# Optimization experiments

Measured on AMD Instinct MI355X. Metric: run time of the kernel, lower is better.

## Reference

```python
import jax, jax.numpy as jnp
import numpy as np

NUM_HEADS = 8
FOCUSING_FACTOR = 3
EPS = 1e-6


def _focus(x, f):
    # focusing: x**f, renormalized to keep the original L2 norm per token
    n = jnp.linalg.norm(x, axis=-1, keepdims=True)
    xp = x ** f
    return xp / jnp.linalg.norm(xp, axis=-1, keepdims=True) * n


def _split_heads(x, h):
    # b n (h c) -> (b h) n c
    b, n, C = x.shape
    return x.reshape(b, n, h, C // h).transpose(0, 2, 1, 3).reshape(b * h, n, C // h)


def setup_inputs() -> dict:
    key = jax.random.key(0)
    ks = jax.random.split(key, 9)
    B, Nq, Nkv, C = 8, 4096, 4096, 512
    query = jax.random.normal(ks[0], (B, Nq, C), jnp.float32)
    key_in = jax.random.normal(ks[1], (B, Nkv, C), jnp.float32)
    value = jax.random.normal(ks[2], (B, Nkv, C), jnp.float32)
    Wq = jax.random.normal(ks[3], (C, C), jnp.float32) * 0.02
    Wk = jax.random.normal(ks[4], (C, C), jnp.float32) * 0.02
    Wv = jax.random.normal(ks[5], (C, C), jnp.float32) * 0.02
    Wp = jax.random.normal(ks[6], (C, C), jnp.float32) * 0.02
    bp = jnp.zeros((C,), jnp.float32)
    scale = jax.random.normal(ks[7], (1, 1, C), jnp.float32) * 0.02
    return {"query": query, "key_in": key_in, "value": value,
            "Wq": Wq, "Wk": Wk, "Wv": Wv, "Wp": Wp, "bp": bp,
            "scale": scale, "H": 64, "W": 64}


def reference(query, key_in, value, Wq, Wk, Wv, Wp, bp, scale, H, W):
    B, N, C = query.shape
    h = NUM_HEADS
    # projections (qkv_bias=False)
    q = jax.nn.relu(query @ Wq) + EPS
    k = jax.nn.relu(key_in @ Wk) + EPS
    v = value @ Wv
    s = jax.nn.softplus(scale)  # [1,1,C]
    q = q / s
    k = k / s
    q = _focus(q, FOCUSING_FACTOR)
    k = _focus(k, FOCUSING_FACTOR)
    q = _split_heads(q, h)  # [(B h), N, c]
    k = _split_heads(k, h)
    v = _split_heads(v, h)
    # z-normalizer: 1 / (q . sum_j k_j)
    z = 1.0 / (jnp.einsum('bic,bc->bi', q, k.sum(axis=1)) + EPS)
    # O(n) kv-aggregation path (i*j*(c+d) > c*d*(i+j) for these shapes)
    kv = jnp.einsum('bjc,bjd->bcd', k, v)
    x = jnp.einsum('bic,bcd,bi->bid', q, kv, z)
    # (b h) n c -> b n (h c)
    x = x.reshape(B, h, N, C // h).transpose(0, 2, 1, 3).reshape(B, N, C)
    # note: dwc(v) feature_map in the original is dead code (never added to x)
    return x @ Wp + bp
```

## Files before the change

### kernel.cpp

```cpp
#include <hip/hip_runtime.h>
#include <hip/hip_bf16.h>
#include <math.h>

typedef __attribute__((ext_vector_type(8))) short short8;
typedef __attribute__((ext_vector_type(4))) float f32x4;

#define MFMA16x16x32(A,B,C) __builtin_amdgcn_mfma_f32_16x16x32_bf16((A),(B),(C),0,0,0)

__device__ __forceinline__ short f2b(float x) {
  __hip_bfloat16 h = __float2bfloat16(x);
  short s; __builtin_memcpy(&s, &h, 2); return s;
}
__device__ __forceinline__ float b2f(short s) {
  __hip_bfloat16 h; __builtin_memcpy(&h, &s, 2); return __bfloat162float(h);
}

__global__ __launch_bounds__(256)
void prep_kernel(const float* __restrict__ Wq, const float* __restrict__ Wk,
                 const float* __restrict__ Wv, const float* __restrict__ Wp,
                 const float* __restrict__ scale,
                 short* __restrict__ wpack, float* __restrict__ spls)
{
  const int b = blockIdx.x;
  const int t = threadIdx.x;
  if (b == 64) {
    for (int i = t; i < 512; i += 256) {
      float x = scale[i];
      spls[i] = (x > 20.f) ? x : log1pf(expf(x));
    }
    return;
  }
  const float* Ws[4] = {Wq, Wk, Wv, Wp};
  const int w = b >> 4, kf16 = b & 15;
  const float* W = Ws[w];
  short* dst = wpack + (size_t)w * (512 * 512);
  __shared__ short lds[32 * 512];
  for (int i = 0; i < 64; ++i) {
    int idx = i * 256 + t;
    int r = idx >> 9, c = idx & 511;
    lds[idx] = f2b(W[(size_t)(kf16 * 32 + r) * 512 + c]);
  }
  __syncthreads();
  for (int s = 0; s < 8; ++s) {
    int slot = s * 256 + t;
    int nf = slot >> 6, l = slot & 63;
    int n = nf * 16 + (l & 15);
    int k0 = 8 * (l >> 4);
    short8 v;
#pragma unroll
    for (int jj = 0; jj < 8; ++jj) v[jj] = lds[(k0 + jj) * 512 + n];
    *(short8*)(dst + ((size_t)(kf16 * 32 + nf) * 64 + l) * 8) = v;
  }
}

template<int MODE>
__global__ __launch_bounds__(512, 2)
void proj_kernel(const void* __restrict__ Xv, const short* __restrict__ wpk,
                 const float* __restrict__ spls, short* __restrict__ outp,
                 const float* __restrict__ bp, float* __restrict__ outf)
{
  __shared__ char smem[65536];
  __shared__ float pnorm[2][8][64];
  __shared__ float facs[64];
  short* tile = (short*)smem;
  const int t = threadIdx.x;
  const int lane = t & 63;
  const int wid = t >> 6;
  const int g = lane >> 4;
  const int cl = lane & 15;
  const int rb = blockIdx.x << 6;
  const int sr = t >> 3;
  const int sc = t & 7;

  const float* Xf = (const float*)Xv;
  const short* Xb = (const short*)Xv;
  const short8* wp8 = (const short8*)wpk;

  {
    char* dst = smem + sr * 272 + sc * 32;
    if (MODE < 3) {
      const float* src = Xf + (size_t)(rb + sr) * 512 + sc * 16;
      f32x4 a0 = *(const f32x4*)(src);
      f32x4 a1 = *(const f32x4*)(src + 4);
      f32x4 a2 = *(const f32x4*)(src + 8);
      f32x4 a3 = *(const f32x4*)(src + 12);
      short8 v0, v1;
#pragma unroll
      for (int j = 0; j < 4; ++j) {
        v0[j] = f2b(a0[j]); v0[4 + j] = f2b(a1[j]);
        v1[j] = f2b(a2[j]); v1[4 + j] = f2b(a3[j]);
      }
      *(short8*)dst = v0; *(short8*)(dst + 16) = v1;
    } else {
      const short* src = Xb + (size_t)(rb + sr) * 512 + sc * 16;
      *(short8*)dst = *(const short8*)src;
      *(short8*)(dst + 16) = *(const short8*)(src + 8);
    }
  }
  f32x4 zero4 = {0.f, 0.f, 0.f, 0.f};
  f32x4 acc[4][4];
#pragma unroll
  for (int rf = 0; rf < 4; ++rf)
#pragma unroll
    for (int cf = 0; cf < 4; ++cf) acc[rf][cf] = zero4;

  short8 bcur[4], bnxt[4];
#pragma unroll
  for (int cf = 0; cf < 4; ++cf)
    bcur[cf] = wp8[((size_t)(wid * 4 + cf)) * 64 + lane];
  __syncthreads();

#pragma unroll
  for (int s = 0; s < 4; ++s) {
    char* cur = smem + (s & 1) * 17408;
    char* nxt = smem + ((s + 1) & 1) * 17408;
    f32x4 rA0, rA1, rA2, rA3;
    short8 rB0, rB1;
    if (s < 3) {
      if (MODE < 3) {
        const float* src = Xf + (size_t)(rb + sr) * 512 + (s + 1) * 128 + sc * 16;
        rA0 = *(const f32x4*)(src);
        rA1 = *(const f32x4*)(src + 4);
        rA2 = *(const f32x4*)(src + 8);
        rA3 = *(const f32x4*)(src + 12);
      } else {
        const short* src = Xb + (size_t)(rb + sr) * 512 + (s + 1) * 128 + sc * 16;
        rB0 = *(const short8*)src;
        rB1 = *(const short8*)(src + 8);
      }
    }
#pragma unroll
    for (int kfl = 0; kfl < 4; ++kfl) {
      const int kf = s * 4 + kfl;
      if (kf < 15) {
#pragma unroll
        for (int cf = 0; cf < 4; ++cf)
          bnxt[cf] = wp8[((size_t)((kf + 1) * 32 + wid * 4 + cf)) * 64 + lane];
      }
      short8 af[4];
#pragma unroll
      for (int rf = 0; rf < 4; ++rf)
        af[rf] = *(const short8*)(cur + (rf * 16 + cl) * 272 + kfl * 64 + 16 * g);
#pragma unroll
      for (int rf = 0; rf < 4; ++rf)
#pragma unroll
        for (int cf = 0; cf < 4; ++cf)
          acc[rf][cf] = MFMA16x16x32(af[rf], bcur[cf], acc[rf][cf]);
      if (kf < 15) {
#pragma unroll
        for (int cf = 0; cf < 4; ++cf) bcur[cf] = bnxt[cf];
      }
    }
    if (s < 3) {
      char* dst = nxt + sr * 272 + sc * 32;
      short8 v0, v1;
      if (MODE < 3) {
#pragma unroll
        for (int j = 0; j < 4; ++j) {
          v0[j] = f2b(rA0[j]); v0[4 + j] = f2b(rA1[j]);
          v1[j] = f2b(rA2[j]); v1[4 + j] = f2b(rA3[j]);
        }
      } else { v0 = rB0; v1 = rB1; }
      *(short8*)dst = v0; *(short8*)(dst + 16) = v1;
      __syncthreads();
    }
  }

  if (MODE == 3) {
#pragma unroll
    for (int rf = 0; rf < 4; ++rf)
#pragma unroll
      for (int cf = 0; cf < 4; ++cf) {
        int c = wid * 64 + cf * 16 + cl;
        float bv = bp[c];
#pragma unroll
        for (int j = 0; j < 4; ++j)
          outf[(size_t)(rb + rf * 16 + 4 * g + j) * 512 + c] = acc[rf][cf][j] + bv;
      }
    return;
  }

  if (MODE < 2) {
    float sp_inv[4];
#pragma unroll
    for (int cf = 0; cf < 4; ++cf) sp_inv[cf] = 1.f / spls[wid * 64 + cf * 16 + cl];
    float p2[4][4], p6[4][4];
#pragma unroll
    for (int rf = 0; rf < 4; ++rf)
#pragma unroll
      for (int j = 0; j < 4; ++j) { p2[rf][j] = 0.f; p6[rf][j] = 0.f; }
#pragma unroll
    for (int rf = 0; rf < 4; ++rf)
#pragma unroll
      for (int cf = 0; cf < 4; ++cf)
#pragma unroll
        for (int j = 0; j < 4; ++j) {
          float v = acc[rf][cf][j];
          v = fmaxf(v, 0.f) + 1e-6f;
          v *= sp_inv[cf];
          acc[rf][cf][j] = v;
          float v2 = v * v;
          p2[rf][j] += v2;
          p6[rf][j] += v2 * v2 * v2;
        }
#pragma unroll
    for (int m = 1; m < 16; m <<= 1) {
#pragma unroll
      for (int rf = 0; rf < 4; ++rf)
#pragma unroll
        for (int j = 0; j < 4; ++j) {
          p2[rf][j] += __shfl_xor(p2[rf][j], m, 64);
          p6[rf][j] += __shfl_xor(p6[rf][j], m, 64);
        }
    }
    if (cl == 0) {
#pragma unroll
      for (int rf = 0; rf < 4; ++rf)
#pragma unroll
        for (int j = 0; j < 4; ++j) {
          pnorm[0][wid][rf * 16 + 4 * g + j] = p2[rf][j];
          pnorm[1][wid][rf * 16 + 4 * g + j] = p6[rf][j];
        }
    }
    __syncthreads();
    if (t < 64) {
      float a = 0.f, b = 0.f;
#pragma unroll
      for (int w = 0; w < 8; ++w) { a += pnorm[0][w][t]; b += pnorm[1][w][t]; }
      facs[t] = sqrtf(a / b);
    }
    __syncthreads();
    float fac[4][4];
#pragma unroll
    for (int rf = 0; rf < 4; ++rf)
#pragma unroll
      for (int j = 0; j < 4; ++j) fac[rf][j] = facs[rf * 16 + 4 * g + j];
#pragma unroll
    for (int rf = 0; rf < 4; ++rf)
#pragma unroll
      for (int cf = 0; cf < 4; ++cf)
#pragma unroll
        for (int j = 0; j < 4; ++j) {
          float v = acc[rf][cf][j];
          float o = v * v * v * fac[rf][j];
          int r = rf * 16 + 4 * g + j;
          int c = wid * 64 + cf * 16 + cl;
          int byteoff = (r * 1024 + c * 2) ^ ((r & 7) << 4);
          *(short*)((char*)tile + byteoff) = f2b(o);
        }
  } else {
    __syncthreads();
#pragma unroll
    for (int rf = 0; rf < 4; ++rf)
#pragma unroll
      for (int cf = 0; cf < 4; ++cf)
#pragma unroll
        for (int j = 0; j < 4; ++j) {
          int r = rf * 16 + 4 * g + j;
          int c = wid * 64 + cf * 16 + cl;
          int byteoff = (r * 1024 + c * 2) ^ ((r & 7) << 4);
          *(short*)((char*)tile + byteoff) = f2b(acc[rf][cf][j]);
        }
  }
  __syncthreads();

  if (MODE == 0) {
    const int r = t >> 3;
    const int c8 = t & 7;
#pragma unroll
    for (int s = 0; s < 8; ++s) {
      int ci = c8 + 8 * s;
      int byteoff = (r * 1024 + ci * 16) ^ ((r & 7) << 4);
      short8 v = *(const short8*)((const char*)tile + byteoff);
      *(short8*)(outp + (size_t)(rb + r) * 512 + ci * 8) = v;
    }
  } else {
    const int l = lane;
    const int batch = rb >> 12;
    const int jf_base = (rb & 4095) >> 5;
#pragma unroll
    for (int s = 0; s < 8; ++s) {
      int fidx = wid * 8 + s;
      int jf = fidx >> 5;
      int cf = fidx & 31;
      int c = cf * 16 + (l & 15);
      int j0 = jf * 32 + 8 * (l >> 4);
      short8 v;
#pragma unroll
      for (int jj = 0; jj < 8; ++jj) {
        int j = j0 + jj;
        int byteoff = (j * 1024 + c * 2) ^ ((j & 7) << 4);
        v[jj] = *(const short*)((const char*)tile + byteoff);
      }
      int bh = batch * 8 + (cf >> 2);
      int cfh = cf & 3;
      int jfg = jf_base + jf;
      *(short8*)(outp + (((size_t)(bh * 128 + jfg) * 4 + cfh) * 64 + l) * 8) = v;
    }
  }
}

__global__ __launch_bounds__(256)
void kv_kernel(const short* __restrict__ kpack, const short* __restrict__ vpack,
               float* __restrict__ pKV, float* __restrict__ pKS)
{
  __shared__ float red[4][64 * 64];
  __shared__ float ksacc[64];
  const int t = threadIdx.x;
  const int lane = t & 63;
  const int w = t >> 6;
  const int g = lane >> 4;
  const int cl = lane & 15;
  const int bh = blockIdx.x >> 3;
  const int sp = blockIdx.x & 7;
  if (t < 64) ksacc[t] = 0.f;
  __syncthreads();

  f32x4 zero4 = {0.f, 0.f, 0.f, 0.f};
  f32x4 acc[4][4];
#pragma unroll
  for (int df = 0; df < 4; ++df)
#pragma unroll
    for (int cf = 0; cf < 4; ++cf) acc[df][cf] = zero4;
  float ks[4] = {0.f, 0.f, 0.f, 0.f};
  const short8* kp = (const short8*)kpack;
  const short8* vp = (const short8*)vpack;

#pragma unroll
  for (int i = 0; i < 4; ++i) {
    int jfg = sp * 16 + w * 4 + i;
    size_t base = ((size_t)bh * 128 + jfg) * 4 * 64;
    short8 afr[4], bfr[4];
#pragma unroll
    for (int f = 0; f < 4; ++f) {
      afr[f] = vp[base + (size_t)f * 64 + lane];
      bfr[f] = kp[base + (size_t)f * 64 + lane];
    }
#pragma unroll
    for (int cf = 0; cf < 4; ++cf) {
      float s = 0.f;
#pragma unroll
      for (int jj = 0; jj < 8; ++jj) s += b2f(bfr[cf][jj]);
      ks[cf] += s;
    }
#pragma unroll
    for (int df = 0; df < 4; ++df)
#pragma unroll
      for (int cf = 0; cf < 4; ++cf)
        acc[df][cf] = MFMA16x16x32(afr[df], bfr[cf], acc[df][cf]);
  }

#pragma unroll
  for (int cf = 0; cf < 4; ++cf) {
    ks[cf] += __shfl_xor(ks[cf], 16, 64);
    ks[cf] += __shfl_xor(ks[cf], 32, 64);
  }
  if (lane < 16) {
#pragma unroll
    for (int cf = 0; cf < 4; ++cf) atomicAdd(&ksacc[cf * 16 + lane], ks[cf]);
  }

#pragma unroll
  for (int df = 0; df < 4; ++df)
#pragma unroll
    for (int cf = 0; cf < 4; ++cf)
#pragma unroll
      for (int j = 0; j < 4; ++j)
        red[w][(df * 16 + 4 * g + j) * 64 + cf * 16 + cl] = acc[df][cf][j];
  __syncthreads();

  float* dkv = pKV + (size_t)blockIdx.x * 4096;
  for (int i = t; i < 4096; i += 256)
    dkv[i] = red[0][i] + red[1][i] + red[2][i] + red[3][i];
  if (t < 64) pKS[(size_t)blockIdx.x * 64 + t] = ksacc[t];
}

__global__ __launch_bounds__(256)
void kv_reduce(const float* __restrict__ pKV, const float* __restrict__ pKS,
               short* __restrict__ kvT, float* __restrict__ ksum)
{
  const int bh = blockIdx.x;
  const int t = threadIdx.x;
  for (int i = t; i < 4096; i += 256) {
    float s = 0.f;
#pragma unroll
    for (int sp = 0; sp < 8; ++sp) s += pKV[(size_t)(bh * 8 + sp) * 4096 + i];
    kvT[(size_t)bh * 4096 + i] = f2b(s);
  }
  if (t < 64) {
    float s = 0.f;
#pragma unroll
    for (int sp = 0; sp < 8; ++sp) s += pKS[(size_t)(bh * 8 + sp) * 64 + t];
    ksum[bh * 64 + t] = s;
  }
}

__global__ __launch_bounds__(512)
void x_kernel(const short* __restrict__ qf, const short* __restrict__ kvT,
              const float* __restrict__ ksum, short* __restrict__ xout)
{
  __shared__ short xt[64 * 512];
  __shared__ float ksb[512];
  __shared__ float zb[64 * 8];
  const int t = threadIdx.x;
  const int lane = t & 63;
  const int wid = t >> 6;
  const int wr = wid >> 1;
  const int wc = wid & 1;
  const int g = lane >> 4;
  const int cl = lane & 15;
  const int rb = blockIdx.x << 6;
  const int batch = rb >> 12;

  ksb[t] = ksum[batch * 512 + t];
  __syncthreads();

  {
    int r = t >> 3, h = t & 7;
    const short8* qrow = (const short8*)(qf + (size_t)(rb + r) * 512 + h * 64);
    float d = 0.f;
#pragma unroll
    for (int c8 = 0; c8 < 8; ++c8) {
      short8 qv = qrow[c8];
#pragma unroll
      for (int jj = 0; jj < 8; ++jj) d += b2f(qv[jj]) * ksb[h * 64 + c8 * 8 + jj];
    }
    zb[r * 8 + h] = 1.f / (d + 1e-6f);
  }
  __syncthreads();

  f32x4 zero4 = {0.f, 0.f, 0.f, 0.f};
  f32x4 xacc[16];
#pragma unroll
  for (int i = 0; i < 16; ++i) xacc[i] = zero4;

  const short8* q8 = (const short8*)qf;
  const size_t qrowbase = (size_t)(rb + wr * 16 + cl) * 64;
#pragma unroll
  for (int hh = 0; hh < 4; ++hh) {
    int h = wc * 4 + hh;
    short8 af0 = q8[qrowbase + h * 8 + g];
    short8 af1 = q8[qrowbase + h * 8 + 4 + g];
    const short8* kv8 = (const short8*)kvT + ((size_t)(batch * 8 + h)) * 512;
#pragma unroll
    for (int nfl = 0; nfl < 4; ++nfl) {
      short8 b0 = kv8[(size_t)(nfl * 16 + cl) * 8 + g];
      short8 b1 = kv8[(size_t)(nfl * 16 + cl) * 8 + 4 + g];
      int nf = hh * 4 + nfl;
      xacc[nf] = MFMA16x16x32(af0, b0, xacc[nf]);
      xacc[nf] = MFMA16x16x32(af1, b1, xacc[nf]);
    }
  }
#pragma unroll
  for (int hh = 0; hh < 4; ++hh) {
    int h = wc * 4 + hh;
    float z4[4];
#pragma unroll
    for (int j = 0; j < 4; ++j) z4[j] = zb[(wr * 16 + 4 * g + j) * 8 + h];
#pragma unroll
    for (int nfl = 0; nfl < 4; ++nfl) {
      int nf = hh * 4 + nfl;
#pragma unroll
      for (int j = 0; j < 4; ++j) {
        float xv = xacc[nf][j] * z4[j];
        int r = wr * 16 + 4 * g + j;
        int c = wc * 256 + nf * 16 + cl;
        int byteoff = (r * 1024 + c * 2) ^ ((r & 7) << 4);
        *(short*)((char*)xt + byteoff) = f2b(xv);
      }
    }
  }
  __syncthreads();

  const int r = t >> 3;
  const int c8 = t & 7;
#pragma unroll
  for (int s = 0; s < 8; ++s) {
    int ci = c8 + 8 * s;
    int byteoff = (r * 1024 + ci * 16) ^ ((r & 7) << 4);
    short8 v = *(const short8*)((const char*)xt + byteoff);
    *(short8*)(xout + (size_t)(rb + r) * 512 + ci * 8) = v;
  }
}

extern "C" void kernel_launch(void* const* d_in, const int* in_sizes, int n_in,
                              void* d_out, int out_size, void* d_ws, size_t ws_size,
                              hipStream_t stream)
{
  const float* query  = (const float*)d_in[0];
  const float* key_in = (const float*)d_in[1];
  const float* value  = (const float*)d_in[2];
  const float* Wq     = (const float*)d_in[3];
  const float* Wk     = (const float*)d_in[4];
  const float* Wv     = (const float*)d_in[5];
  const float* Wp     = (const float*)d_in[6];
  const float* bp     = (const float*)d_in[7];
  const float* scale  = (const float*)d_in[8];
  float* out = (float*)d_out;

  char* ws = (char*)d_ws;
  size_t off = 0;
  auto alloc = [&](size_t bytes) -> void* {
    void* p = ws + off;
    off += (bytes + 255) & ~(size_t)255;
    return p;
  };
  float* spls  = (float*)alloc(512 * 4);
  short* wpack = (short*)alloc((size_t)4 * 512 * 512 * 2);
  short* qf    = (short*)alloc((size_t)32768 * 512 * 2);
  short* kpack = (short*)alloc((size_t)32768 * 512 * 2);
  short* vpack = (short*)alloc((size_t)32768 * 512 * 2);
  float* pKV   = (float*)alloc((size_t)512 * 4096 * 4);
  float* pKS   = (float*)alloc((size_t)512 * 64 * 4);
  short* kvT   = (short*)alloc((size_t)64 * 4096 * 2);
  float* ksum  = (float*)alloc((size_t)64 * 64 * 4);
  short* xbuf  = kpack;

  prep_kernel<<<65, 256, 0, stream>>>(Wq, Wk, Wv, Wp, scale, wpack, spls);
  proj_kernel<0><<<512, 512, 0, stream>>>(query,  wpack + (size_t)0 * 512 * 512, spls, qf,    nullptr, nullptr);
  proj_kernel<1><<<512, 512, 0, stream>>>(key_in, wpack + (size_t)1 * 512 * 512, spls, kpack, nullptr, nullptr);
  proj_kernel<2><<<512, 512, 0, stream>>>(value,  wpack + (size_t)2 * 512 * 512, spls, vpack, nullptr, nullptr);
  kv_kernel<<<512, 256, 0, stream>>>(kpack, vpack, pKV, pKS);
  kv_reduce<<<64, 256, 0, stream>>>(pKV, pKS, kvT, ksum);
  x_kernel<<<512, 512, 0, stream>>>(qf, kvT, ksum, xbuf);
  proj_kernel<3><<<512, 512, 0, stream>>>(xbuf, wpack + (size_t)3 * 512 * 512, spls, nullptr, bp, out);
}
```

Measured before the change: 212.3 us.

## Fuse Q/K/V projections into one launch with 128-row tiles and fragment-packed LDS

```diff
diff --git a/kernel.cpp b/kernel.cpp
--- a/kernel.cpp
+++ b/kernel.cpp
@@ -53,33 +53,41 @@
   }
 }
 
-template<int MODE>
-__global__ __launch_bounds__(512, 2)
-void proj_kernel(const void* __restrict__ Xv, const short* __restrict__ wpk,
-                 const float* __restrict__ spls, short* __restrict__ outp,
-                 const float* __restrict__ bp, float* __restrict__ outf)
+__global__ __launch_bounds__(1024, 4)
+void proj_big(const float* __restrict__ Aq, const float* __restrict__ Ak,
+              const float* __restrict__ Av, const short* __restrict__ Ax,
+              const short* __restrict__ wpack, const float* __restrict__ spls,
+              short* __restrict__ qf, short* __restrict__ kpack,
+              short* __restrict__ vpack, const float* __restrict__ bp,
+              float* __restrict__ outf, int mode_base)
 {
   __shared__ char smem[65536];
-  __shared__ float pnorm[2][8][64];
-  __shared__ float facs[64];
-  short* tile = (short*)smem;
+  __shared__ float pnorm[2][8][128];
+  __shared__ float facs[128];
+
   const int t = threadIdx.x;
   const int lane = t & 63;
   const int wid = t >> 6;
+  const int wr = wid >> 3;
+  const int wc = wid & 7;
   const int g = lane >> 4;
   const int cl = lane & 15;
-  const int rb = blockIdx.x << 6;
+  const int mode = mode_base + (blockIdx.x >> 8);
+  const int rb = (blockIdx.x & 255) << 7;
   const int sr = t >> 3;
   const int sc = t & 7;
 
-  const float* Xf = (const float*)Xv;
-  const short* Xb = (const short*)Xv;
-  const short8* wp8 = (const short8*)wpk;
+  const float* Af = (mode == 0) ? Aq : (mode == 1) ? Ak : Av;
+  const short8* wp8 = (const short8*)(wpack + (size_t)mode * (512 * 512));
+
+  const int stg_base = (((sc >> 1) * 8 + (sr >> 4)) * 64 + (sr & 15)) * 16;
+  const int stg_g0 = 16 * (2 * (sc & 1)) * 16;
+  const int stg_g1 = 16 * (2 * (sc & 1) + 1) * 16;
 
   {
-    char* dst = smem + sr * 272 + sc * 32;
-    if (MODE < 3) {
-      const float* src = Xf + (size_t)(rb + sr) * 512 + sc * 16;
+    char* dst = smem + stg_base;
+    if (mode < 3) {
+      const float* src = Af + (size_t)(rb + sr) * 512 + sc * 16;
       f32x4 a0 = *(const f32x4*)(src);
       f32x4 a1 = *(const f32x4*)(src + 4);
       f32x4 a2 = *(const f32x4*)(src + 8);
@@ -90,13 +98,14 @@
         v0[j] = f2b(a0[j]); v0[4 + j] = f2b(a1[j]);
         v1[j] = f2b(a2[j]); v1[4 + j] = f2b(a3[j]);
       }
-      *(short8*)dst = v0; *(short8*)(dst + 16) = v1;
+      *(short8*)(dst + stg_g0) = v0; *(short8*)(dst + stg_g1) = v1;
     } else {
-      const short* src = Xb + (size_t)(rb + sr) * 512 + sc * 16;
-      *(short8*)dst = *(const short8*)src;
-      *(short8*)(dst + 16) = *(const short8*)(src + 8);
-    }
-  }
+      const short* src = Ax + (size_t)(rb + sr) * 512 + sc * 16;
+      *(short8*)(dst + stg_g0) = *(const short8*)src;
+      *(short8*)(dst + stg_g1) = *(const short8*)(src + 8);
+    }
+  }
+
   f32x4 zero4 = {0.f, 0.f, 0.f, 0.f};
   f32x4 acc[4][4];
 #pragma unroll
@@ -107,24 +116,23 @@
   short8 bcur[4], bnxt[4];
 #pragma unroll
   for (int cf = 0; cf < 4; ++cf)
-    bcur[cf] = wp8[((size_t)(wid * 4 + cf)) * 64 + lane];
+    bcur[cf] = wp8[((size_t)(wc * 4 + cf)) * 64 + lane];
   __syncthreads();
 
 #pragma unroll
   for (int s = 0; s < 4; ++s) {
-    char* cur = smem + (s & 1) * 17408;
-    char* nxt = smem + ((s + 1) & 1) * 17408;
+    char* cur = smem + (s & 1) * 32768;
     f32x4 rA0, rA1, rA2, rA3;
     short8 rB0, rB1;
     if (s < 3) {
-      if (MODE < 3) {
-        const float* src = Xf + (size_t)(rb + sr) * 512 + (s + 1) * 128 + sc * 16;
+      if (mode < 3) {
+        const float* src = Af + (size_t)(rb + sr) * 512 + (s + 1) * 128 + sc * 16;
         rA0 = *(const f32x4*)(src);
         rA1 = *(const f32x4*)(src + 4);
         rA2 = *(const f32x4*)(src + 8);
         rA3 = *(const f32x4*)(src + 12);
       } else {
-        const short* src = Xb + (size_t)(rb + sr) * 512 + (s + 1) * 128 + sc * 16;
+        const short* src = Ax + (size_t)(rb + sr) * 512 + (s + 1) * 128 + sc * 16;
         rB0 = *(const short8*)src;
         rB1 = *(const short8*)(src + 8);
       }
@@ -135,95 +143,96 @@
       if (kf < 15) {
 #pragma unroll
         for (int cf = 0; cf < 4; ++cf)
-          bnxt[cf] = wp8[((size_t)((kf + 1) * 32 + wid * 4 + cf)) * 64 + lane];
+          bnxt[cf] = wp8[((size_t)((kf + 1) * 32 + wc * 4 + cf)) * 64 + lane];
       }
       short8 af[4];
 #pragma unroll
-      for (int rf = 0; rf < 4; ++rf)
-        af[rf] = *(const short8*)(cur + (rf * 16 + cl) * 272 + kfl * 64 + 16 * g);
-#pragma unroll
-      for (int rf = 0; rf < 4; ++rf)
+      for (int rfl = 0; rfl < 4; ++rfl)
+        af[rfl] = *(const short8*)(cur + ((kfl * 8 + wr * 4 + rfl) * 64 + lane) * 16);
+#pragma unroll
+      for (int rfl = 0; rfl < 4; ++rfl)
 #pragma unroll
         for (int cf = 0; cf < 4; ++cf)
-          acc[rf][cf] = MFMA16x16x32(af[rf], bcur[cf], acc[rf][cf]);
+          acc[rfl][cf] = MFMA16x16x32(af[rfl], bcur[cf], acc[rfl][cf]);
       if (kf < 15) {
 #pragma unroll
         for (int cf = 0; cf < 4; ++cf) bcur[cf] = bnxt[cf];
       }
     }
     if (s < 3) {
-      char* dst = nxt + sr * 272 + sc * 32;
+      char* dst = smem + ((s + 1) & 1) * 32768 + stg_base;
       short8 v0, v1;
-      if (MODE < 3) {
+      if (mode < 3) {
 #pragma unroll
         for (int j = 0; j < 4; ++j) {
           v0[j] = f2b(rA0[j]); v0[4 + j] = f2b(rA1[j]);
           v1[j] = f2b(rA2[j]); v1[4 + j] = f2b(rA3[j]);
         }
       } else { v0 = rB0; v1 = rB1; }
-      *(short8*)dst = v0; *(short8*)(dst + 16) = v1;
+      *(short8*)(dst + stg_g0) = v0; *(short8*)(dst + stg_g1) = v1;
       __syncthreads();
     }
   }
 
-  if (MODE == 3) {
-#pragma unroll
-    for (int rf = 0; rf < 4; ++rf)
+  if (mode == 3) {
+#pragma unroll
+    for (int rfl = 0; rfl < 4; ++rfl)
 #pragma unroll
       for (int cf = 0; cf < 4; ++cf) {
-        int c = wid * 64 + cf * 16 + cl;
+        int c = wc * 64 + cf * 16 + cl;
         float bv = bp[c];
 #pragma unroll
         for (int j = 0; j < 4; ++j)
-          outf[(size_t)(rb + rf * 16 + 4 * g + j) * 512 + c] = acc[rf][cf][j] + bv;
+          outf[(size_t)(rb + wr * 64 + rfl * 16 + 4 * g + j) * 512 + c] = acc[rfl][cf][j] + bv;
       }
     return;
   }
 
-  if (MODE < 2) {
+  if (mode < 2) {
     float sp_inv[4];
 #pragma unroll
-    for (int cf = 0; cf < 4; ++cf) sp_inv[cf] = 1.f / spls[wid * 64 + cf * 16 + cl];
+    for (int cf = 0; cf < 4; ++cf) sp_inv[cf] = 1.f / spls[wc * 64 + cf * 16 + cl];
     float p2[4][4], p6[4][4];
 #pragma unroll
-    for (int rf = 0; rf < 4; ++rf)
-#pragma unroll
-      for (int j = 0; j < 4; ++j) { p2[rf][j] = 0.f; p6[rf][j] = 0.f; }
-#pragma unroll
-    for (int rf = 0; rf < 4; ++rf)
+    for (int rfl = 0; rfl < 4; ++rfl)
+#pragma unroll
+      for (int j = 0; j < 4; ++j) { p2[rfl][j] = 0.f; p6[rfl][j] = 0.f; }
+#pragma unroll
+    for (int rfl = 0; rfl < 4; ++rfl)
 #pragma unroll
       for (int cf = 0; cf < 4; ++cf)
 #pragma unroll
         for (int j = 0; j < 4; ++j) {
-          float v = acc[rf][cf][j];
+          float v = acc[rfl][cf][j];
           v = fmaxf(v, 0.f) + 1e-6f;
           v *= sp_inv[cf];
-          acc[rf][cf][j] = v;
+          acc[rfl][cf][j] = v;
           float v2 = v * v;
-          p2[rf][j] += v2;
-          p6[rf][j] += v2 * v2 * v2;
+          p2[rfl][j] += v2;
+          p6[rfl][j] += v2 * v2 * v2;
         }
 #pragma unroll
     for (int m = 1; m < 16; m <<= 1) {
 #pragma unroll
-      for (int rf = 0; rf < 4; ++rf)
+      for (int rfl = 0; rfl < 4; ++rfl)
 #pragma unroll
         for (int j = 0; j < 4; ++j) {
-          p2[rf][j] += __shfl_xor(p2[rf][j], m, 64);
-          p6[rf][j] += __shfl_xor(p6[rf][j], m, 64);
+          p2[rfl][j] += __shfl_xor(p2[rfl][j], m, 64);
+          p6[rfl][j] += __shfl_xor(p6[rfl][j], m, 64);
         }
     }
     if (cl == 0) {
 #pragma unroll
-      for (int rf = 0; rf < 4; ++rf)
+      for (int rfl = 0; rfl < 4; ++rfl)
 #pragma unroll
         for (int j = 0; j < 4; ++j) {
-          pnorm[0][wid][rf * 16 + 4 * g + j] = p2[rf][j];
-          pnorm[1][wid][rf * 16 + 4 * g + j] = p6[rf][j];
+          int row = wr * 64 + rfl * 16 + 4 * g + j;
+          pnorm[0][wc][row] = p2[rfl][j];
+          pnorm[1][wc][row] = p6[rfl][j];
         }
     }
     __syncthreads();
-    if (t < 64) {
+    if (t < 128) {
       float a = 0.f, b = 0.f;
 #pragma unroll
       for (int w = 0; w < 8; ++w) { a += pnorm[0][w][t]; b += pnorm[1][w][t]; }
@@ -232,70 +241,71 @@
     __syncthreads();
     float fac[4][4];
 #pragma unroll
-    for (int rf = 0; rf < 4; ++rf)
-#pragma unroll
-      for (int j = 0; j < 4; ++j) fac[rf][j] = facs[rf * 16 + 4 * g + j];
-#pragma unroll
-    for (int rf = 0; rf < 4; ++rf)
+    for (int rfl = 0; rfl < 4; ++rfl)
+#pragma unroll
+      for (int j = 0; j < 4; ++j)
+        fac[rfl][j] = facs[wr * 64 + rfl * 16 + 4 * g + j];
+#pragma unroll
+    for (int rfl = 0; rfl < 4; ++rfl)
 #pragma unroll
       for (int cf = 0; cf < 4; ++cf)
 #pragma unroll
         for (int j = 0; j < 4; ++j) {
-          float v = acc[rf][cf][j];
-          float o = v * v * v * fac[rf][j];
-          int r = rf * 16 + 4 * g + j;
-          int c = wid * 64 + cf * 16 + cl;
-          int byteoff = (r * 1024 + c * 2) ^ ((r & 7) << 4);
-          *(short*)((char*)tile + byteoff) = f2b(o);
+          float v = acc[rfl][cf][j];
+          acc[rfl][cf][j] = v * v * v * fac[rfl][j];
         }
-  } else {
+  }
+
+  short* dstp = (mode == 0) ? qf : (mode == 1) ? kpack : vpack;
+  const int batch = rb >> 12;
+#pragma unroll
+  for (int pass = 0; pass < 2; ++pass) {
     __syncthreads();
-#pragma unroll
-    for (int rf = 0; rf < 4; ++rf)
-#pragma unroll
-      for (int cf = 0; cf < 4; ++cf)
-#pragma unroll
-        for (int j = 0; j < 4; ++j) {
-          int r = rf * 16 + 4 * g + j;
-          int c = wid * 64 + cf * 16 + cl;
-          int byteoff = (r * 1024 + c * 2) ^ ((r & 7) << 4);
-          *(short*)((char*)tile + byteoff) = f2b(acc[rf][cf][j]);
+    if (wr == pass) {
+#pragma unroll
+      for (int rfl = 0; rfl < 4; ++rfl)
+#pragma unroll
+        for (int cf = 0; cf < 4; ++cf)
+#pragma unroll
+          for (int j = 0; j < 4; ++j) {
+            int r = rfl * 16 + 4 * g + j;
+            int c = wc * 64 + cf * 16 + cl;
+            int byteoff = (r * 1024 + c * 2) ^ ((r & 7) << 4);
+            *(short*)(smem + byteoff) = f2b(acc[rfl][cf][j]);
+          }
+    }
+    __syncthreads();
+    if (mode == 0) {
+      const int r = t >> 4;
+      const int c16 = t & 15;
+#pragma unroll
+      for (int s2 = 0; s2 < 4; ++s2) {
+        int ci = c16 + 16 * s2;
+        int byteoff = (r * 1024 + ci * 16) ^ ((r & 7) << 4);
+        short8 v = *(const short8*)(smem + byteoff);
+        *(short8*)(dstp + (size_t)(rb + pass * 64 + r) * 512 + ci * 8) = v;
+      }
+    } else {
+      const int jf_base = ((rb & 4095) >> 5) + pass * 2;
+#pragma unroll
+      for (int s2 = 0; s2 < 4; ++s2) {
+        int fidx = wid * 4 + s2;
+        int jf = fidx >> 5;
+        int cf = fidx & 31;
+        int c = cf * 16 + (lane & 15);
+        int j0 = jf * 32 + 8 * (lane >> 4);
+        short8 v;
+#pragma unroll
+        for (int jj = 0; jj < 8; ++jj) {
+          int jrow = j0 + jj;
+          int byteoff = (jrow * 1024 + c * 2) ^ ((jrow & 7) << 4);
+          v[jj] = *(const short*)(smem + byteoff);
         }
-  }
-  __syncthreads();
-
-  if (MODE == 0) {
-    const int r = t >> 3;
-    const int c8 = t & 7;
-#pragma unroll
-    for (int s = 0; s < 8; ++s) {
-      int ci = c8 + 8 * s;
-      int byteoff = (r * 1024 + ci * 16) ^ ((r & 7) << 4);
-      short8 v = *(const short8*)((const char*)tile + byteoff);
-      *(short8*)(outp + (size_t)(rb + r) * 512 + ci * 8) = v;
-    }
-  } else {
-    const int l = lane;
-    const int batch = rb >> 12;
-    const int jf_base = (rb & 4095) >> 5;
-#pragma unroll
-    for (int s = 0; s < 8; ++s) {
-      int fidx = wid * 8 + s;
-      int jf = fidx >> 5;
-      int cf = fidx & 31;
-      int c = cf * 16 + (l & 15);
-      int j0 = jf * 32 + 8 * (l >> 4);
-      short8 v;
-#pragma unroll
-      for (int jj = 0; jj < 8; ++jj) {
-        int j = j0 + jj;
-        int byteoff = (j * 1024 + c * 2) ^ ((j & 7) << 4);
-        v[jj] = *(const short*)((const char*)tile + byteoff);
-      }
-      int bh = batch * 8 + (cf >> 2);
-      int cfh = cf & 3;
-      int jfg = jf_base + jf;
-      *(short8*)(outp + (((size_t)(bh * 128 + jfg) * 4 + cfh) * 64 + l) * 8) = v;
+        int bh = batch * 8 + (cf >> 2);
+        int cfh = cf & 3;
+        int jfg = jf_base + jf;
+        *(short8*)(dstp + (((size_t)(bh * 128 + jfg) * 4 + cfh) * 64 + lane) * 8) = v;
+      }
     }
   }
 }
@@ -517,11 +527,11 @@
   short* xbuf  = kpack;
 
   prep_kernel<<<65, 256, 0, stream>>>(Wq, Wk, Wv, Wp, scale, wpack, spls);
-  proj_kernel<0><<<512, 512, 0, stream>>>(query,  wpack + (size_t)0 * 512 * 512, spls, qf,    nullptr, nullptr);
-  proj_kernel<1><<<512, 512, 0, stream>>>(key_in, wpack + (size_t)1 * 512 * 512, spls, kpack, nullptr, nullptr);
-  proj_kernel<2><<<512, 512, 0, stream>>>(value,  wpack + (size_t)2 * 512 * 512, spls, vpack, nullptr, nullptr);
+  proj_big<<<768, 1024, 0, stream>>>(query, key_in, value, nullptr, wpack, spls,
+                                     qf, kpack, vpack, nullptr, nullptr, 0);
   kv_kernel<<<512, 256, 0, stream>>>(kpack, vpack, pKV, pKS);
   kv_reduce<<<64, 256, 0, stream>>>(pKV, pKS, kvT, ksum);
   x_kernel<<<512, 512, 0, stream>>>(qf, kvT, ksum, xbuf);
-  proj_kernel<3><<<512, 512, 0, stream>>>(xbuf, wpack + (size_t)3 * 512 * 512, spls, nullptr, bp, out);
-}
+  proj_big<<<256, 1024, 0, stream>>>(nullptr, nullptr, nullptr, xbuf, wpack, spls,
+                                     nullptr, nullptr, nullptr, bp, out, 3);
+}
```

Result: slower. 368.9 us (+73.7%).

## Merge Q/K/V projection launches into one grid and stagger K-slice order per block

Applied to the files above, without the earlier changes.

```diff
diff --git a/kernel.cpp b/kernel.cpp
--- a/kernel.cpp
+++ b/kernel.cpp
@@ -53,11 +53,13 @@
   }
 }
 
-template<int MODE>
 __global__ __launch_bounds__(512, 2)
-void proj_kernel(const void* __restrict__ Xv, const short* __restrict__ wpk,
-                 const float* __restrict__ spls, short* __restrict__ outp,
-                 const float* __restrict__ bp, float* __restrict__ outf)
+void proj_kernel(const float* __restrict__ Aq, const float* __restrict__ Ak,
+                 const float* __restrict__ Av, const short* __restrict__ Ax,
+                 const short* __restrict__ wpack, const float* __restrict__ spls,
+                 short* __restrict__ qf, short* __restrict__ kpk,
+                 short* __restrict__ vpk, const float* __restrict__ bp,
+                 float* __restrict__ outf, int mode_base)
 {
   __shared__ char smem[65536];
   __shared__ float pnorm[2][8][64];
@@ -68,18 +70,21 @@
   const int wid = t >> 6;
   const int g = lane >> 4;
   const int cl = lane & 15;
-  const int rb = blockIdx.x << 6;
+  const int bid = blockIdx.x;
+  const int mode = (mode_base == 3) ? 3 : (bid >> 9);
+  const int rb = (bid & 511) << 6;
   const int sr = t >> 3;
   const int sc = t & 7;
-
-  const float* Xf = (const float*)Xv;
-  const short* Xb = (const short*)Xv;
-  const short8* wp8 = (const short8*)wpk;
+  const int r1 = bid & 3;
+  const int r2 = (bid >> 2) & 3;
+
+  const float* Af = (mode == 0) ? Aq : (mode == 1) ? Ak : Av;
+  const short8* wp8 = (const short8*)(wpack + (size_t)mode * (512 * 512));
 
   {
     char* dst = smem + sr * 272 + sc * 32;
-    if (MODE < 3) {
-      const float* src = Xf + (size_t)(rb + sr) * 512 + sc * 16;
+    if (mode < 3) {
+      const float* src = Af + (size_t)(rb + sr) * 512 + r1 * 128 + sc * 16;
       f32x4 a0 = *(const f32x4*)(src);
       f32x4 a1 = *(const f32x4*)(src + 4);
       f32x4 a2 = *(const f32x4*)(src + 8);
@@ -92,7 +97,7 @@
       }
       *(short8*)dst = v0; *(short8*)(dst + 16) = v1;
     } else {
-      const short* src = Xb + (size_t)(rb + sr) * 512 + sc * 16;
+      const short* src = Ax + (size_t)(rb + sr) * 512 + r1 * 128 + sc * 16;
       *(short8*)dst = *(const short8*)src;
       *(short8*)(dst + 16) = *(const short8*)(src + 8);
     }
@@ -105,56 +110,63 @@
     for (int cf = 0; cf < 4; ++cf) acc[rf][cf] = zero4;
 
   short8 bcur[4], bnxt[4];
-#pragma unroll
-  for (int cf = 0; cf < 4; ++cf)
-    bcur[cf] = wp8[((size_t)(wid * 4 + cf)) * 64 + lane];
-  __syncthreads();
-
-#pragma unroll
-  for (int s = 0; s < 4; ++s) {
-    char* cur = smem + (s & 1) * 17408;
-    char* nxt = smem + ((s + 1) & 1) * 17408;
+  {
+    const int kf0 = r1 * 4 + r2;
+#pragma unroll
+    for (int cf = 0; cf < 4; ++cf)
+      bcur[cf] = wp8[((size_t)(kf0 * 32 + wid * 4 + cf)) * 64 + lane];
+  }
+  __syncthreads();
+
+#pragma unroll
+  for (int sl = 0; sl < 4; ++sl) {
+    const int s_phys = (sl + r1) & 3;
+    const int s_next = (s_phys + 1) & 3;
+    char* cur = smem + (sl & 1) * 17408;
     f32x4 rA0, rA1, rA2, rA3;
     short8 rB0, rB1;
-    if (s < 3) {
-      if (MODE < 3) {
-        const float* src = Xf + (size_t)(rb + sr) * 512 + (s + 1) * 128 + sc * 16;
+    if (sl < 3) {
+      if (mode < 3) {
+        const float* src = Af + (size_t)(rb + sr) * 512 + s_next * 128 + sc * 16;
         rA0 = *(const f32x4*)(src);
         rA1 = *(const f32x4*)(src + 4);
         rA2 = *(const f32x4*)(src + 8);
         rA3 = *(const f32x4*)(src + 12);
       } else {
-        const short* src = Xb + (size_t)(rb + sr) * 512 + (s + 1) * 128 + sc * 16;
+        const short* src = Ax + (size_t)(rb + sr) * 512 + s_next * 128 + sc * 16;
         rB0 = *(const short8*)src;
         rB1 = *(const short8*)(src + 8);
       }
     }
 #pragma unroll
-    for (int kfl = 0; kfl < 4; ++kfl) {
-      const int kf = s * 4 + kfl;
-      if (kf < 15) {
+    for (int kl = 0; kl < 4; ++kl) {
+      const int k_phys = (kl + r2) & 3;
+      const bool last = (sl == 3) && (kl == 3);
+      if (!last) {
+        const int kf_n = (kl < 3) ? (s_phys * 4 + ((kl + 1 + r2) & 3))
+                                  : (((s_phys + 1) & 3) * 4 + r2);
 #pragma unroll
         for (int cf = 0; cf < 4; ++cf)
-          bnxt[cf] = wp8[((size_t)((kf + 1) * 32 + wid * 4 + cf)) * 64 + lane];
+          bnxt[cf] = wp8[((size_t)(kf_n * 32 + wid * 4 + cf)) * 64 + lane];
       }
       short8 af[4];
 #pragma unroll
       for (int rf = 0; rf < 4; ++rf)
-        af[rf] = *(const short8*)(cur + (rf * 16 + cl) * 272 + kfl * 64 + 16 * g);
+        af[rf] = *(const short8*)(cur + (rf * 16 + cl) * 272 + k_phys * 64 + 16 * g);
 #pragma unroll
       for (int rf = 0; rf < 4; ++rf)
 #pragma unroll
         for (int cf = 0; cf < 4; ++cf)
           acc[rf][cf] = MFMA16x16x32(af[rf], bcur[cf], acc[rf][cf]);
-      if (kf < 15) {
+      if (!last) {
 #pragma unroll
         for (int cf = 0; cf < 4; ++cf) bcur[cf] = bnxt[cf];
       }
     }
-    if (s < 3) {
-      char* dst = nxt + sr * 272 + sc * 32;
+    if (sl < 3) {
+      char* dst = smem + ((sl + 1) & 1) * 17408 + sr * 272 + sc * 32;
       short8 v0, v1;
-      if (MODE < 3) {
+      if (mode < 3) {
 #pragma unroll
         for (int j = 0; j < 4; ++j) {
           v0[j] = f2b(rA0[j]); v0[4 + j] = f2b(rA1[j]);
@@ -166,7 +178,7 @@
     }
   }
 
-  if (MODE == 3) {
+  if (mode == 3) {
 #pragma unroll
     for (int rf = 0; rf < 4; ++rf)
 #pragma unroll
@@ -180,7 +192,7 @@
     return;
   }
 
-  if (MODE < 2) {
+  if (mode < 2) {
     float sp_inv[4];
 #pragma unroll
     for (int cf = 0; cf < 4; ++cf) sp_inv[cf] = 1.f / spls[wid * 64 + cf * 16 + cl];
@@ -264,7 +276,7 @@
   }
   __syncthreads();
 
-  if (MODE == 0) {
+  if (mode == 0) {
     const int r = t >> 3;
     const int c8 = t & 7;
 #pragma unroll
@@ -272,9 +284,10 @@
       int ci = c8 + 8 * s;
       int byteoff = (r * 1024 + ci * 16) ^ ((r & 7) << 4);
       short8 v = *(const short8*)((const char*)tile + byteoff);
-      *(short8*)(outp + (size_t)(rb + r) * 512 + ci * 8) = v;
+      *(short8*)(qf + (size_t)(rb + r) * 512 + ci * 8) = v;
     }
   } else {
+    short* dstp = (mode == 1) ? kpk : vpk;
     const int l = lane;
     const int batch = rb >> 12;
     const int jf_base = (rb & 4095) >> 5;
@@ -295,7 +308,7 @@
       int bh = batch * 8 + (cf >> 2);
       int cfh = cf & 3;
       int jfg = jf_base + jf;
-      *(short8*)(outp + (((size_t)(bh * 128 + jfg) * 4 + cfh) * 64 + l) * 8) = v;
+      *(short8*)(dstp + (((size_t)(bh * 128 + jfg) * 4 + cfh) * 64 + l) * 8) = v;
     }
   }
 }
@@ -517,11 +530,11 @@
   short* xbuf  = kpack;
 
   prep_kernel<<<65, 256, 0, stream>>>(Wq, Wk, Wv, Wp, scale, wpack, spls);
-  proj_kernel<0><<<512, 512, 0, stream>>>(query,  wpack + (size_t)0 * 512 * 512, spls, qf,    nullptr, nullptr);
-  proj_kernel<1><<<512, 512, 0, stream>>>(key_in, wpack + (size_t)1 * 512 * 512, spls, kpack, nullptr, nullptr);
-  proj_kernel<2><<<512, 512, 0, stream>>>(value,  wpack + (size_t)2 * 512 * 512, spls, vpack, nullptr, nullptr);
+  proj_kernel<<<1536, 512, 0, stream>>>(query, key_in, value, nullptr, wpack, spls,
+                                        qf, kpack, vpack, nullptr, nullptr, 0);
   kv_kernel<<<512, 256, 0, stream>>>(kpack, vpack, pKV, pKS);
   kv_reduce<<<64, 256, 0, stream>>>(pKV, pKS, kvT, ksum);
   x_kernel<<<512, 512, 0, stream>>>(qf, kvT, ksum, xbuf);
-  proj_kernel<3><<<512, 512, 0, stream>>>(xbuf, wpack + (size_t)3 * 512 * 512, spls, nullptr, bp, out);
-}
+  proj_kernel<<<512, 512, 0, stream>>>(nullptr, nullptr, nullptr, xbuf, wpack, spls,
+                                       nullptr, nullptr, nullptr, bp, out, 3);
+}
```

Measured after the change: 206.4 us. 2.8% less time.
